# Kernel optimization log

Measured on AMD Instinct MI355X. Metric: run time of the kernel, lower is better.

Reference implementation:

```python
import jax, jax.numpy as jnp
import numpy as np

NUM_EMBED = 8192
EMBED_DIM = 64
BETA = 0.25
B, H, W = 8, 64, 64


def setup_inputs() -> dict:
    key = jax.random.key(0)
    k1, k2 = jax.random.split(key)
    z = jax.random.normal(k1, (B, EMBED_DIM, H, W), dtype=jnp.float32)
    # matches nn.Embedding init: uniform(-1/num_embed, 1/num_embed)
    embed_weight = jax.random.uniform(
        k2, (NUM_EMBED, EMBED_DIM), dtype=jnp.float32,
        minval=-1.0 / NUM_EMBED, maxval=1.0 / NUM_EMBED)
    return {"z": z, "embed_weight": embed_weight}


def _l2_normalize(x, eps=1e-12):
    # F.normalize(dim=1): x / max(||x||, eps)
    n = jnp.sqrt(jnp.sum(x * x, axis=1, keepdims=True))
    return x / jnp.maximum(n, eps)


def reference(z, embed_weight):
    num_embed = embed_weight.shape[0]
    zc = jnp.transpose(z, (0, 2, 3, 1))              # b h w c
    zf = zc.reshape(-1, embed_weight.shape[1])        # [N, d]
    # cosine distance (z side detached in original)
    zn = jax.lax.stop_gradient(_l2_normalize(zf))
    cn = _l2_normalize(embed_weight)
    dist = jnp.einsum('nd,kd->nk', zn, cn)            # [N, K]
    # sort(dim=1)[:, -1] == argmax along codes
    idx = jnp.argmax(dist, axis=1)                    # [N]
    # one-hot @ codebook == gather (identical math, no NxK one-hot)
    z_q = embed_weight[idx].reshape(zc.shape)         # b h w c
    loss = (BETA * jnp.mean((jax.lax.stop_gradient(z_q) - zc) ** 2)
            + jnp.mean((z_q - jax.lax.stop_gradient(zc)) ** 2))
    # straight-through estimator
    z_q_ste = zc + jax.lax.stop_gradient(z_q - zc)
    z_q_out = jnp.transpose(z_q_ste, (0, 3, 1, 2))    # b c h w
    bin_count = jnp.bincount(idx, length=num_embed)   # eval-mode bincount
    return z_q_out, loss, idx, bin_count
```

## Files before the change

### kernel.cpp

```cpp
#include <hip/hip_runtime.h>

#define NUM_EMBED 8192
#define DIMC 64
#define HW 4096
#define NQ 32768
#define ZQ_SIZE  2097152
#define LOSS_OFF 2097152
#define IDX_OFF  2097153
#define BIN_OFF  2129921
#define EPS 1.5e-4f

#define WS_B      0
#define WS_INV    2097152
#define WS_CNT    2129920
#define WS_LIST   2129936
#define WS_PART   2261008

typedef unsigned int  uint;
typedef unsigned short ushort;
typedef __attribute__((ext_vector_type(8))) short short8;
typedef __attribute__((ext_vector_type(4))) float float4_;
typedef __attribute__((ext_vector_type(2))) float float2_;

__device__ inline ushort f2bf(float f) {
    uint u = __float_as_uint(f);
    return (ushort)((u + 0x7FFFu + ((u >> 16) & 1u)) >> 16);
}
__device__ inline float bf2f(ushort h) { return __uint_as_float(((uint)h) << 16); }

__global__ __launch_bounds__(256) void vq_prep_b(const float* __restrict__ ew,
        ushort* __restrict__ Bp, float* __restrict__ invn,
        float* __restrict__ out, int* __restrict__ cnt)
{
    const int gi = blockIdx.x * 256 + threadIdx.x;
    if (gi < NUM_EMBED) out[BIN_OFF + gi] = 0.0f;
    if (gi == 0) { out[LOSS_OFF] = 0.0f; *cnt = 0; }

    const int ln  = threadIdx.x & 63;
    const int wv  = threadIdx.x >> 6;
    const int row = blockIdx.x * 4 + wv;
    float v = ew[row * 64 + ln];
    float s = v * v;
    #pragma unroll
    for (int off = 1; off < 64; off <<= 1) s += __shfl_xor(s, off, 64);
    float rinv = 1.0f / fmaxf(sqrtf(s), 1e-12f);
    float cn = v * rinv;
    ushort hi = f2bf(cn);
    ushort lo = f2bf(cn - bf2f(hi));
    Bp[row * 128 + ln]      = hi;
    Bp[row * 128 + 64 + ln] = lo;
    if (ln == 0) invn[row] = rinv;
}

__global__ __launch_bounds__(256, 2) void vq_main(const float* __restrict__ z,
        const ushort* __restrict__ Bp, const float* __restrict__ ew,
        float* __restrict__ out, int* __restrict__ cnt, int* __restrict__ list)
{
    __shared__ __align__(16) ushort qtile[64 * 136];
    __shared__ float msc[4 * 64 * 3];
    __shared__ int   ibuf[64];
    __shared__ int   ubuf[64];
    __shared__ float lred[4];

    const int tid = threadIdx.x;
    const int ln  = tid & 63;
    const int w   = tid >> 6;
    const int lm  = ln & 15;
    const int h   = ln >> 4;
    const int h8  = h * 8;

    const int q0  = blockIdx.x * 64;
    const int b   = q0 >> 12;
    const int hw0 = q0 & 4095;

    {
        const int qr = tid & 63;
        const int cb = (tid >> 6) * 16;
        const float* zb = z + (size_t)b * (DIMC * HW) + hw0 + qr;
        #pragma unroll
        for (int i = 0; i < 16; ++i) {
            int c = cb + i;
            float f = zb[(size_t)c * HW];
            ushort hi = f2bf(f);
            ushort lo = f2bf(f - bf2f(hi));
            qtile[qr * 136 + c]      = hi;
            qtile[qr * 136 + 64 + c] = lo;
        }
    }
    __syncthreads();

    short8 qh0[4], qh1[4], ql0[4], ql1[4];
    #pragma unroll
    for (int qt = 0; qt < 4; ++qt) {
        const ushort* r = &qtile[(qt * 16 + lm) * 136 + h8];
        qh0[qt] = *(const short8*)(r);
        qh1[qt] = *(const short8*)(r + 32);
        ql0[qt] = *(const short8*)(r + 64);
        ql1[qt] = *(const short8*)(r + 96);
    }

    float v1[4], v2[4]; int i1[4];
    #pragma unroll
    for (int qt = 0; qt < 4; ++qt) { v1[qt] = -3e38f; v2[qt] = -3e38f; i1[qt] = 0; }

    const ushort* gp = Bp + (size_t)(w * 16 + lm) * 128 + h8;
    const int wh = w * 16 + h * 4;

    auto compute = [&](short8 ch0, short8 ch1, short8 cl0, short8 cl1, int t) {
        float4_ s[4];
        #pragma unroll
        for (int qt = 0; qt < 4; ++qt) {
            float4_ a  = (float4_){0.f, 0.f, 0.f, 0.f};
            float4_ bb = (float4_){0.f, 0.f, 0.f, 0.f};
            a  = __builtin_amdgcn_mfma_f32_16x16x32_bf16(ch0, qh0[qt], a, 0, 0, 0);
            bb = __builtin_amdgcn_mfma_f32_16x16x32_bf16(ch0, ql0[qt], bb, 0, 0, 0);
            a  = __builtin_amdgcn_mfma_f32_16x16x32_bf16(ch1, qh1[qt], a, 0, 0, 0);
            bb = __builtin_amdgcn_mfma_f32_16x16x32_bf16(ch1, ql1[qt], bb, 0, 0, 0);
            a  = __builtin_amdgcn_mfma_f32_16x16x32_bf16(cl0, ql0[qt], a, 0, 0, 0);
            bb = __builtin_amdgcn_mfma_f32_16x16x32_bf16(cl0, qh0[qt], bb, 0, 0, 0);
            a  = __builtin_amdgcn_mfma_f32_16x16x32_bf16(cl1, ql1[qt], a, 0, 0, 0);
            bb = __builtin_amdgcn_mfma_f32_16x16x32_bf16(cl1, qh1[qt], bb, 0, 0, 0);
            s[qt] = a + bb;
        }
        const int cb2 = t * 64 + wh;
        #pragma unroll
        for (int rr = 0; rr < 4; ++rr) {
            int code = cb2 + rr;
            #pragma unroll
            for (int qt = 0; qt < 4; ++qt) {
                float v = s[qt][rr];
                v2[qt] = __builtin_amdgcn_fmed3f(v, v1[qt], v2[qt]);
                bool gt = v > v1[qt];
                v1[qt] = fmaxf(v1[qt], v);
                i1[qt] = gt ? code : i1[qt];
            }
        }
    };

    short8 A0, A1, A2, A3, B0, B1, B2, B3;
#define LDF(d0, d1, d2, d3, T) { const ushort* p = gp + (size_t)(T) * 8192; \
        d0 = *(const short8*)(p);      d1 = *(const short8*)(p + 32);       \
        d2 = *(const short8*)(p + 64); d3 = *(const short8*)(p + 96); }

    LDF(A0, A1, A2, A3, 0)
    #pragma unroll 1
    for (int t = 0; t < 128; t += 2) {
        LDF(B0, B1, B2, B3, t + 1)
        compute(A0, A1, A2, A3, t);
        if (t < 126) LDF(A0, A1, A2, A3, t + 2)
        compute(B0, B1, B2, B3, t + 1);
    }
#undef LDF

    #pragma unroll
    for (int m = 16; m <= 32; m <<= 1) {
        #pragma unroll
        for (int qt = 0; qt < 4; ++qt) {
            float ov1 = __shfl_xor(v1[qt], m, 64);
            int   oi1 = __shfl_xor(i1[qt], m, 64);
            float ov2 = __shfl_xor(v2[qt], m, 64);
            float nv2 = fmaxf(fminf(v1[qt], ov1), fmaxf(v2[qt], ov2));
            bool tk = ov1 > v1[qt];
            v1[qt] = tk ? ov1 : v1[qt];
            i1[qt] = tk ? oi1 : i1[qt];
            v2[qt] = nv2;
        }
    }

    if (h == 0) {
        #pragma unroll
        for (int qt = 0; qt < 4; ++qt) {
            int o = (w * 64 + qt * 16 + lm) * 3;
            msc[o] = v1[qt];
            ((int*)msc)[o + 1] = i1[qt];
            msc[o + 2] = v2[qt];
        }
    }
    __syncthreads();
    if (tid < 64) {
        float fv1 = -3e38f, fv2 = -3e38f; int fi = 0;
        #pragma unroll
        for (int wv = 0; wv < 4; ++wv) {
            int o = (wv * 64 + tid) * 3;
            float a1 = msc[o], a2 = msc[o + 2];
            int   ai = ((int*)msc)[o + 1];
            float nv2 = fmaxf(fminf(fv1, a1), fmaxf(fv2, a2));
            bool tk = a1 > fv1;
            fv1 = tk ? a1 : fv1;
            fi  = tk ? ai : fi;
            fv2 = nv2;
        }
        int q = q0 + tid;
        out[IDX_OFF + q] = (float)fi;
        int unc = (fv1 - fv2 <= EPS) ? 1 : 0;
        ibuf[tid] = fi;
        ubuf[tid] = unc;
        if (unc) {
            int s = atomicAdd(cnt, 1);
            list[s] = q;
        } else {
            atomicAdd(&out[BIN_OFF + fi], 1.0f);
        }
    }
    __syncthreads();

    {
        const int qL = tid & 63;
        const int cq = tid >> 6;
        int fi  = ibuf[qL];
        int unc = ubuf[qL];
        float lsum = 0.f;
        if (!unc) {
            const float4_* wr4 = (const float4_*)(ew + (size_t)fi * 64) + cq * 4;
            const float* zsrc = z   + (size_t)b * (DIMC * HW) + hw0 + qL;
            float*       zq   = out + (size_t)b * (DIMC * HW) + hw0 + qL;
            #pragma unroll
            for (int j = 0; j < 4; ++j) {
                float4_ wv4 = wr4[j];
                #pragma unroll
                for (int e = 0; e < 4; ++e) {
                    int c = cq * 16 + j * 4 + e;
                    float zv = zsrc[(size_t)c * HW];
                    zq[(size_t)c * HW] = wv4[e];
                    float dd = wv4[e] - zv;
                    lsum = fmaf(dd, dd, lsum);
                }
            }
        }
        #pragma unroll
        for (int off = 32; off; off >>= 1) lsum += __shfl_down(lsum, off, 64);
        if (ln == 0) lred[w] = lsum;
    }
    __syncthreads();
    if (tid == 0) {
        float s = lred[0] + lred[1] + lred[2] + lred[3];
        atomicAdd(&out[LOSS_OFF], s * (1.25f / (float)ZQ_SIZE));
    }
}

__global__ __launch_bounds__(256) void vq_rescan_a(const float* __restrict__ z,
        const float* __restrict__ ew, const float* __restrict__ invn,
        const int* __restrict__ cnt, const int* __restrict__ list,
        float2_* __restrict__ part, int cap)
{
    __shared__ float zsh[64];
    __shared__ float wbv[4]; __shared__ int wbi[4];
    const int tid   = threadIdx.x;
    const int ln    = tid & 63;
    const int wv    = tid >> 6;
    const int chunk = blockIdx.x & 15;
    const int n = *cnt;
    const int nc = (n < cap) ? n : cap;
    for (int u = blockIdx.x >> 4; u < nc; u += 256) {
        int q = list[u];
        int b = q >> 12, hw = q & 4095;
        if (tid < 64) zsh[tid] = z[(size_t)b * (DIMC * HW) + (size_t)tid * HW + hw];
        __syncthreads();

        const int k1 = chunk * 512 + tid;
        const int k2 = k1 + 256;
        const float4_* r1 = (const float4_*)(ew + (size_t)k1 * 64);
        const float4_* r2 = (const float4_*)(ew + (size_t)k2 * 64);
        float a0 = 0.f, a1 = 0.f, b0 = 0.f, b1 = 0.f;
        #pragma unroll
        for (int c4 = 0; c4 < 16; ++c4) {
            float4_ va = r1[c4], vb = r2[c4];
            float z0 = zsh[c4 * 4 + 0], z1 = zsh[c4 * 4 + 1];
            float z2 = zsh[c4 * 4 + 2], z3 = zsh[c4 * 4 + 3];
            a0 = fmaf(va[0], z0, a0); a1 = fmaf(va[1], z1, a1);
            a0 = fmaf(va[2], z2, a0); a1 = fmaf(va[3], z3, a1);
            b0 = fmaf(vb[0], z0, b0); b1 = fmaf(vb[1], z1, b1);
            b0 = fmaf(vb[2], z2, b0); b1 = fmaf(vb[3], z3, b1);
        }
        float d1 = (a0 + a1) * invn[k1];
        float d2 = (b0 + b1) * invn[k2];
        float bv = (d1 >= d2) ? d1 : d2;
        int   bk = (d1 >= d2) ? k1 : k2;
        #pragma unroll
        for (int m = 1; m < 64; m <<= 1) {
            float ov = __shfl_xor(bv, m, 64);
            int   oi = __shfl_xor(bk, m, 64);
            if (ov > bv || (ov == bv && oi < bk)) { bv = ov; bk = oi; }
        }
        if (ln == 0) { wbv[wv] = bv; wbi[wv] = bk; }
        __syncthreads();
        if (tid == 0) {
            float fb = wbv[0]; int fi = wbi[0];
            #pragma unroll
            for (int w2 = 1; w2 < 4; ++w2) {
                if (wbv[w2] > fb || (wbv[w2] == fb && wbi[w2] < fi)) {
                    fb = wbv[w2]; fi = wbi[w2];
                }
            }
            float2_ p; p[0] = fb; p[1] = __int_as_float(fi);
            part[u * 16 + chunk] = p;
        }
        __syncthreads();
    }
}

__global__ __launch_bounds__(64) void vq_rescan_b(const float* __restrict__ z,
        const float* __restrict__ ew, const float* __restrict__ invn,
        const int* __restrict__ cnt, const int* __restrict__ list,
        const float2_* __restrict__ part, int cap, float* __restrict__ out)
{
    __shared__ float zsh[64];
    __shared__ int sfi;
    const int tid = threadIdx.x;
    const int n = *cnt;
    for (int u = blockIdx.x; u < n; u += gridDim.x) {
        int q = list[u];
        int b = q >> 12, hw = q & 4095;
        zsh[tid] = z[(size_t)b * (DIMC * HW) + (size_t)tid * HW + hw];
        __syncthreads();
        if (tid == 0) {
            float fb = -3e38f; int fi = 0;
            if (u < cap) {
                for (int c = 0; c < 16; ++c) {
                    float2_ p = part[u * 16 + c];
                    float pv = p[0]; int pk = __float_as_int(p[1]);
                    if (pv > fb || (pv == fb && pk < fi)) { fb = pv; fi = pk; }
                }
            } else {
                for (int k = 0; k < NUM_EMBED; ++k) {
                    const float* row = ew + (size_t)k * 64;
                    float s = 0.f;
                    for (int c = 0; c < 64; ++c) s = fmaf(row[c], zsh[c], s);
                    s *= invn[k];
                    if (s > fb) { fb = s; fi = k; }
                }
            }
            out[IDX_OFF + q] = (float)fi;
            atomicAdd(&out[BIN_OFF + fi], 1.0f);
            sfi = fi;
        }
        __syncthreads();
        {
            int fi = sfi;
            float wvv = ew[(size_t)fi * 64 + tid];
            out[(size_t)b * (DIMC * HW) + (size_t)tid * HW + hw] = wvv;
            float dd = wvv - zsh[tid];
            float lsum = dd * dd;
            #pragma unroll
            for (int off = 32; off; off >>= 1) lsum += __shfl_down(lsum, off, 64);
            if (tid == 0) atomicAdd(&out[LOSS_OFF], lsum * (1.25f / (float)ZQ_SIZE));
        }
        __syncthreads();
    }
}

extern "C" void kernel_launch(void* const* d_in, const int* in_sizes, int n_in,
                              void* d_out, int out_size, void* d_ws, size_t ws_size,
                              hipStream_t stream) {
    const float* z  = (const float*)d_in[0];
    const float* ew = (const float*)d_in[1];
    float* out = (float*)d_out;
    char* ws = (char*)d_ws;
    ushort* Bp    = (ushort*)(ws + WS_B);
    float* invn   = (float*)(ws + WS_INV);
    int* cnt      = (int*)(ws + WS_CNT);
    int* list     = (int*)(ws + WS_LIST);
    float2_* part = (float2_*)(ws + WS_PART);
    int cap = 0;
    if (ws_size > WS_PART + 128) {
        size_t avail = (ws_size - WS_PART) / (16 * sizeof(float2_));
        cap = (int)(avail < 4096 ? avail : 4096);
    }

    vq_prep_b<<<NUM_EMBED / 4, 256, 0, stream>>>(ew, Bp, invn, out, cnt);
    vq_main<<<NQ / 64, 256, 0, stream>>>(z, Bp, ew, out, cnt, list);
    vq_rescan_a<<<4096, 256, 0, stream>>>(z, ew, invn, cnt, list, part, cap);
    vq_rescan_b<<<2048, 64, 0, stream>>>(z, ew, invn, cnt, list, part, cap, out);
}
```

Baseline: 202.6 us.

## Drop low-low bf16 split product, software-pipeline MFMA and top-2, shrink rescan grids

The split-bf16 dot product now uses six MFMAs per tile instead of eight by dropping the low*low terms and using one accumulator chain. The loop is reorganised so the MFMAs for the next code tile are issued before the top-2 selection of the previous one, which overlaps matrix work with VALU compares. To cover the larger approximation error, the ambiguity threshold EPS is raised, which likely sends more queries to the exact fp32 rescan. The rescan kernels are launched with fewer blocks and a matching loop stride.

```diff
diff --git a/kernel.cpp b/kernel.cpp
--- a/kernel.cpp
+++ b/kernel.cpp
@@ -8,7 +8,7 @@
 #define LOSS_OFF 2097152
 #define IDX_OFF  2097153
 #define BIN_OFF  2129921
-#define EPS 1.5e-4f
+#define EPS 2.5e-4f
 
 #define WS_B      0
 #define WS_INV    2097152
@@ -106,22 +106,20 @@
     const ushort* gp = Bp + (size_t)(w * 16 + lm) * 128 + h8;
     const int wh = w * 16 + h * 4;
 
-    auto compute = [&](short8 ch0, short8 ch1, short8 cl0, short8 cl1, int t) {
-        float4_ s[4];
+    auto mfma3 = [&](short8 c0, short8 c1, short8 d0, short8 d1, float4_* s) {
         #pragma unroll
         for (int qt = 0; qt < 4; ++qt) {
-            float4_ a  = (float4_){0.f, 0.f, 0.f, 0.f};
-            float4_ bb = (float4_){0.f, 0.f, 0.f, 0.f};
-            a  = __builtin_amdgcn_mfma_f32_16x16x32_bf16(ch0, qh0[qt], a, 0, 0, 0);
-            bb = __builtin_amdgcn_mfma_f32_16x16x32_bf16(ch0, ql0[qt], bb, 0, 0, 0);
-            a  = __builtin_amdgcn_mfma_f32_16x16x32_bf16(ch1, qh1[qt], a, 0, 0, 0);
-            bb = __builtin_amdgcn_mfma_f32_16x16x32_bf16(ch1, ql1[qt], bb, 0, 0, 0);
-            a  = __builtin_amdgcn_mfma_f32_16x16x32_bf16(cl0, ql0[qt], a, 0, 0, 0);
-            bb = __builtin_amdgcn_mfma_f32_16x16x32_bf16(cl0, qh0[qt], bb, 0, 0, 0);
-            a  = __builtin_amdgcn_mfma_f32_16x16x32_bf16(cl1, ql1[qt], a, 0, 0, 0);
-            bb = __builtin_amdgcn_mfma_f32_16x16x32_bf16(cl1, qh1[qt], bb, 0, 0, 0);
-            s[qt] = a + bb;
-        }
+            float4_ a = (float4_){0.f, 0.f, 0.f, 0.f};
+            a = __builtin_amdgcn_mfma_f32_16x16x32_bf16(c0, qh0[qt], a, 0, 0, 0);
+            a = __builtin_amdgcn_mfma_f32_16x16x32_bf16(c1, qh1[qt], a, 0, 0, 0);
+            a = __builtin_amdgcn_mfma_f32_16x16x32_bf16(c0, ql0[qt], a, 0, 0, 0);
+            a = __builtin_amdgcn_mfma_f32_16x16x32_bf16(c1, ql1[qt], a, 0, 0, 0);
+            a = __builtin_amdgcn_mfma_f32_16x16x32_bf16(d0, qh0[qt], a, 0, 0, 0);
+            a = __builtin_amdgcn_mfma_f32_16x16x32_bf16(d1, qh1[qt], a, 0, 0, 0);
+            s[qt] = a;
+        }
+    };
+    auto top2 = [&](const float4_* s, int t) {
         const int cb2 = t * 64 + wh;
         #pragma unroll
         for (int rr = 0; rr < 4; ++rr) {
@@ -138,17 +136,24 @@
     };
 
     short8 A0, A1, A2, A3, B0, B1, B2, B3;
+    float4_ sP[4], sQ[4];
 #define LDF(d0, d1, d2, d3, T) { const ushort* p = gp + (size_t)(T) * 8192; \
         d0 = *(const short8*)(p);      d1 = *(const short8*)(p + 32);       \
         d2 = *(const short8*)(p + 64); d3 = *(const short8*)(p + 96); }
 
     LDF(A0, A1, A2, A3, 0)
+    LDF(B0, B1, B2, B3, 1)
+    mfma3(A0, A1, A2, A3, sP);
     #pragma unroll 1
     for (int t = 0; t < 128; t += 2) {
-        LDF(B0, B1, B2, B3, t + 1)
-        compute(A0, A1, A2, A3, t);
-        if (t < 126) LDF(A0, A1, A2, A3, t + 2)
-        compute(B0, B1, B2, B3, t + 1);
+        mfma3(B0, B1, B2, B3, sQ);
+        if (t + 2 < 128) LDF(A0, A1, A2, A3, t + 2)
+        top2(sP, t);
+        if (t + 2 < 128) {
+            mfma3(A0, A1, A2, A3, sP);
+            if (t + 3 < 128) LDF(B0, B1, B2, B3, t + 3)
+        }
+        top2(sQ, t + 1);
     }
 #undef LDF
 
@@ -251,7 +256,7 @@
     const int chunk = blockIdx.x & 15;
     const int n = *cnt;
     const int nc = (n < cap) ? n : cap;
-    for (int u = blockIdx.x >> 4; u < nc; u += 256) {
+    for (int u = blockIdx.x >> 4; u < nc; u += 64) {
         int q = list[u];
         int b = q >> 12, hw = q & 4095;
         if (tid < 64) zsh[tid] = z[(size_t)b * (DIMC * HW) + (size_t)tid * HW + hw];
@@ -369,6 +374,6 @@
 
     vq_prep_b<<<NUM_EMBED / 4, 256, 0, stream>>>(ew, Bp, invn, out, cnt);
     vq_main<<<NQ / 64, 256, 0, stream>>>(z, Bp, ew, out, cnt, list);
-    vq_rescan_a<<<4096, 256, 0, stream>>>(z, ew, invn, cnt, list, part, cap);
-    vq_rescan_b<<<2048, 64, 0, stream>>>(z, ew, invn, cnt, list, part, cap, out);
-}
+    vq_rescan_a<<<1024, 256, 0, stream>>>(z, ew, invn, cnt, list, part, cap);
+    vq_rescan_b<<<256, 64, 0, stream>>>(z, ew, invn, cnt, list, part, cap, out);
+}
```

Result: no change. 205.1 us (+1.3%).
